# Optimization experiments

Measured on AMD Instinct MI355X. Metric: run time of the kernel, lower is better.

## Reference

```python
import jax, jax.numpy as jnp
import numpy as np

B, S, UNITS = 32, 4096, 512

def setup_inputs() -> dict:
    key = jax.random.key(0)
    ks = jax.random.split(key, 5)
    scale = 1.0 / np.sqrt(UNITS)
    return {
        "s_prev": jax.random.normal(ks[0], (B, UNITS), dtype=jnp.float32),
        "hidden_states": jax.random.normal(ks[1], (B, S, UNITS), dtype=jnp.float32),
        "Ww": jax.random.normal(ks[2], (UNITS, UNITS), dtype=jnp.float32) * scale,
        "Wb": jnp.zeros((UNITS,), dtype=jnp.float32),
        "Uw": jax.random.normal(ks[3], (UNITS, UNITS), dtype=jnp.float32) * scale,
        "Ub": jnp.zeros((UNITS,), dtype=jnp.float32),
        "Vw": jax.random.normal(ks[4], (UNITS, 1), dtype=jnp.float32) * scale,
        "Vb": jnp.zeros((1,), dtype=jnp.float32),
    }

def reference(s_prev, hidden_states, Ww, Wb, Uw, Ub, Vw, Vb):
    # W(s_prev): [B, 1, U] so it broadcasts over seq axis
    W_s = (s_prev @ Ww + Wb)[:, None, :]
    # U(hidden_states): [B, S, U]
    U_h = jnp.einsum('bsu,uv->bsv', hidden_states, Uw) + Ub
    score = jnp.tanh(W_s + U_h)                      # [B, S, U]
    logits = jnp.einsum('bsu,uo->bso', score, Vw) + Vb  # [B, S, 1]
    weights = jax.nn.softmax(logits, axis=1)         # softmax over seq axis
    context = jnp.sum(weights * hidden_states, axis=1)  # [B, U]
    return (context, weights)
```

## Files before the change

kernel.cpp:

```cpp
#include <hip/hip_runtime.h>
#include <hip/hip_bf16.h>

#define UNITS 512
#define SEQ   4096
#define BATCH 32

typedef __attribute__((ext_vector_type(8))) __bf16 bf16x8;
typedef __attribute__((ext_vector_type(4))) __bf16 bf16x4;
typedef __attribute__((ext_vector_type(4))) float  f32x4;

__global__ void k_transpose(const float* __restrict__ Uw, __bf16* __restrict__ UwT) {
    __shared__ float tile[32][33];
    int k0 = blockIdx.x * 32, n0 = blockIdx.y * 32;
    int tx = threadIdx.x, ty = threadIdx.y;
#pragma unroll
    for (int i = 0; i < 4; i++) {
        int k = k0 + ty + i * 8;
        tile[ty + i * 8][tx] = Uw[k * UNITS + n0 + tx];
    }
    __syncthreads();
#pragma unroll
    for (int i = 0; i < 4; i++) {
        int n = n0 + ty + i * 8;
        UwT[n * UNITS + k0 + tx] = (__bf16)tile[tx][ty + i * 8];
    }
}

__global__ void k_wsrow(const float* __restrict__ s_prev, const float* __restrict__ Ww,
                        const float* __restrict__ Wb, const float* __restrict__ Ub,
                        float* __restrict__ ws_Ws) {
    __shared__ float sp[UNITS];
    int b = blockIdx.x, t = threadIdx.x;
    sp[t] = s_prev[b * UNITS + t];
    sp[t + 256] = s_prev[b * UNITS + t + 256];
    __syncthreads();
    float a0 = Wb[t] + Ub[t];
    float a1 = Wb[t + 256] + Ub[t + 256];
#pragma unroll 8
    for (int u = 0; u < UNITS; u++) {
        float s = sp[u];
        a0 += s * Ww[u * UNITS + t];
        a1 += s * Ww[u * UNITS + t + 256];
    }
    ws_Ws[b * UNITS + t] = a0;
    ws_Ws[b * UNITS + t + 256] = a1;
}

#define BM 64
#define BN 256
#define BK 32
#define NSTEP (UNITS / BK)

__launch_bounds__(512)
__global__ void k_logits(const float* __restrict__ hidden, const __bf16* __restrict__ UwT,
                         const float* __restrict__ wsu, const float* __restrict__ Vw,
                         float* __restrict__ lpart) {
    __shared__ __bf16 Ab[2][BM * BK];
    __shared__ __bf16 Bb[2][BN * BK];
    __shared__ float  lred[BM][4];

    const int t = threadIdx.x;
    const int lane = t & 63, wv = t >> 6;
    const int wm = wv >> 2, wn = wv & 3;
    const int l15 = lane & 15, l4 = lane >> 4;
    const int gx = blockIdx.x;
    const int m0 = blockIdx.y * BM;
    const int b  = m0 >> 12;
    const int n0 = gx * BN;

    f32x4 acc[2][4];
#pragma unroll
    for (int i = 0; i < 2; i++)
#pragma unroll
        for (int j = 0; j < 4; j++) acc[i][j] = (f32x4){0.f, 0.f, 0.f, 0.f};

    auto stageA = [&](int buf, int kk) {
        int r = t >> 3, c4 = (t & 7) * 4;
        const float4 v = *(const float4*)(hidden + (size_t)(m0 + r) * UNITS + kk + c4);
        bf16x4 bv;
        bv[0] = (__bf16)v.x; bv[1] = (__bf16)v.y; bv[2] = (__bf16)v.z; bv[3] = (__bf16)v.w;
        *(bf16x4*)(&Ab[buf][r * BK + c4]) = bv;
    };
    auto stageB = [&](int buf, int kk) {
#pragma unroll
        for (int j = 0; j < 2; j++) {
            int idx = wv * 2 + j;
            int nb = idx * 16;
            int n = nb + (lane >> 2);
            int ke = (lane & 3) * 8;
            const __bf16* gp = UwT + (size_t)(n0 + n) * UNITS + kk + ke;
            __builtin_amdgcn_global_load_lds(
                (const __attribute__((address_space(1))) void*)gp,
                (__attribute__((address_space(3))) void*)(&Bb[buf][nb * BK]),
                16, 0, 0);
        }
    };

    stageA(0, 0);
    stageB(0, 0);

#pragma unroll 2
    for (int step = 0; step < NSTEP; ++step) {
        __syncthreads();
        const int cur = step & 1;
        if (step + 1 < NSTEP) {
            stageA(cur ^ 1, (step + 1) * BK);
            stageB(cur ^ 1, (step + 1) * BK);
        }
        bf16x8 a[2], bfr[4];
#pragma unroll
        for (int fi = 0; fi < 2; fi++)
            a[fi] = *(const bf16x8*)(&Ab[cur][(wm * 32 + fi * 16 + l15) * BK + l4 * 8]);
#pragma unroll
        for (int fj = 0; fj < 4; fj++)
            bfr[fj] = *(const bf16x8*)(&Bb[cur][(wn * 64 + fj * 16 + l15) * BK + l4 * 8]);
#pragma unroll
        for (int fi = 0; fi < 2; fi++)
#pragma unroll
            for (int fj = 0; fj < 4; fj++)
                acc[fi][fj] = __builtin_amdgcn_mfma_f32_16x16x32_bf16(a[fi], bfr[fj], acc[fi][fj], 0, 0, 0);
    }

    float wsub[4], vww[4];
#pragma unroll
    for (int fj = 0; fj < 4; fj++) {
        int n = n0 + wn * 64 + fj * 16 + l15;
        wsub[fj] = wsu[b * UNITS + n];
        vww[fj]  = Vw[n];
    }
#pragma unroll
    for (int fi = 0; fi < 2; fi++) {
#pragma unroll
        for (int r = 0; r < 4; r++) {
            float p = 0.f;
#pragma unroll
            for (int fj = 0; fj < 4; fj++) {
                float x = acc[fi][fj][r] + wsub[fj];
                float e = __expf(2.f * x);
                p += vww[fj] * (1.f - 2.f / (e + 1.f));
            }
#pragma unroll
            for (int off = 1; off < 16; off <<= 1) p += __shfl_xor(p, off);
            if (l15 == 0) lred[wm * 32 + fi * 16 + l4 * 4 + r][wn] = p;
        }
    }
    __syncthreads();
    if (t < BM) {
        float s = lred[t][0] + lred[t][1] + lred[t][2] + lred[t][3];
        lpart[(size_t)(m0 + t) * 2 + gx] = s;
    }
}

__global__ void k_softmax(const float* __restrict__ lpart, float* __restrict__ wout) {
    __shared__ float ebuf[SEQ];
    __shared__ float red[8];
    int b = blockIdx.x, t = threadIdx.x;
    int lane = t & 63, wv = t >> 6;
    float m = -1e30f;
#pragma unroll
    for (int i = 0; i < 16; i++) {
        int s = t + i * 256;
        size_t idx = ((size_t)b * SEQ + s) * 2;
        float l = lpart[idx] + lpart[idx + 1];
        ebuf[s] = l;
        m = fmaxf(m, l);
    }
#pragma unroll
    for (int off = 32; off >= 1; off >>= 1) m = fmaxf(m, __shfl_xor(m, off));
    if (lane == 0) red[wv] = m;
    __syncthreads();
    m = fmaxf(fmaxf(red[0], red[1]), fmaxf(red[2], red[3]));
    float zs = 0.f;
#pragma unroll
    for (int i = 0; i < 16; i++) {
        int s = t + i * 256;
        float e = __expf(ebuf[s] - m);
        ebuf[s] = e;
        zs += e;
    }
#pragma unroll
    for (int off = 32; off >= 1; off >>= 1) zs += __shfl_xor(zs, off);
    __syncthreads();
    if (lane == 0) red[wv] = zs;
    __syncthreads();
    float inv = 1.f / (red[0] + red[1] + red[2] + red[3]);
#pragma unroll
    for (int i = 0; i < 16; i++) {
        int s = t + i * 256;
        wout[(size_t)b * SEQ + s] = ebuf[s] * inv;
    }
}

__global__ void k_ctxpart(const float* __restrict__ hidden, const float* __restrict__ wout,
                          float* __restrict__ part) {
    int b = blockIdx.y, c = blockIdx.x, t = threadIdx.x;
    const float* w = wout + (size_t)b * SEQ + c * 128;
    const float* h = hidden + ((size_t)b * SEQ + c * 128) * UNITS;
    float2 acc = make_float2(0.f, 0.f);
#pragma unroll 4
    for (int s = 0; s < 128; s++) {
        float ww = w[s];
        float2 v = ((const float2*)(h + (size_t)s * UNITS))[t];
        acc.x += ww * v.x;
        acc.y += ww * v.y;
    }
    ((float2*)(part + ((size_t)(b * 32 + c)) * UNITS))[t] = acc;
}

__global__ void k_ctxreduce(const float* __restrict__ part, float* __restrict__ ctx) {
    int b = blockIdx.x, t = threadIdx.x;
    float s = 0.f;
#pragma unroll
    for (int c = 0; c < 32; c++) s += part[((size_t)(b * 32 + c)) * UNITS + t];
    ctx[(size_t)b * UNITS + t] = s;
}

extern "C" void kernel_launch(void* const* d_in, const int* in_sizes, int n_in,
                              void* d_out, int out_size, void* d_ws, size_t ws_size,
                              hipStream_t stream) {
    const float* s_prev = (const float*)d_in[0];
    const float* hidden = (const float*)d_in[1];
    const float* Ww     = (const float*)d_in[2];
    const float* Wb     = (const float*)d_in[3];
    const float* Uw     = (const float*)d_in[4];
    const float* Ub     = (const float*)d_in[5];
    const float* Vw     = (const float*)d_in[6];

    float* out  = (float*)d_out;
    float* ctx  = out;
    float* wout = out + BATCH * UNITS;

    float* wsf   = (float*)d_ws;
    float* ws_Ws = wsf;
    float* ws_lp = ws_Ws + BATCH * UNITS;
    float* ws_cp = ws_lp + (size_t)BATCH * SEQ * 2;
    __bf16* UwT  = (__bf16*)(ws_cp + (size_t)BATCH * 32 * UNITS);

    k_transpose<<<dim3(16, 16), dim3(32, 8), 0, stream>>>(Uw, UwT);
    k_wsrow<<<dim3(32), dim3(256), 0, stream>>>(s_prev, Ww, Wb, Ub, ws_Ws);
    k_logits<<<dim3(2, 2048), dim3(512), 0, stream>>>(hidden, UwT, ws_Ws, Vw, ws_lp);
    k_softmax<<<dim3(32), dim3(256), 0, stream>>>(ws_lp, wout);
    k_ctxpart<<<dim3(32, 32), dim3(256), 0, stream>>>(hidden, wout, ws_cp);
    k_ctxreduce<<<dim3(32), dim3(512), 0, stream>>>(ws_cp, ctx);
}
```

Baseline: 225.4 us.

## Double logits M-tile, pre-tile and swizzle Uw, use XOR-swizzled LDS layouts

Doubles the logits GEMM M tile to 128 rows, so each wave computes a 4x4 grid of MFMA fragments and the grid halves. The transposed bf16 Uw is now prepacked into per-k-step, XOR-swizzled 16KB tiles, so the B stage becomes contiguous global_load_lds copies. The A tile is stored with the same swizzle, using 8-element bf16 writes. This is meant to cut redundant reads of hidden, LDS bank conflicts and address arithmetic, at the cost of more registers per thread (launch bounds of 4) and more LDS.

```diff
diff --git a/kernel.cpp b/kernel.cpp
--- a/kernel.cpp
+++ b/kernel.cpp
@@ -6,24 +6,23 @@
 #define BATCH 32
 
 typedef __attribute__((ext_vector_type(8))) __bf16 bf16x8;
-typedef __attribute__((ext_vector_type(4))) __bf16 bf16x4;
 typedef __attribute__((ext_vector_type(4))) float  f32x4;
 
-__global__ void k_transpose(const float* __restrict__ Uw, __bf16* __restrict__ UwT) {
-    __shared__ float tile[32][33];
-    int k0 = blockIdx.x * 32, n0 = blockIdx.y * 32;
-    int tx = threadIdx.x, ty = threadIdx.y;
-#pragma unroll
-    for (int i = 0; i < 4; i++) {
-        int k = k0 + ty + i * 8;
-        tile[ty + i * 8][tx] = Uw[k * UNITS + n0 + tx];
-    }
-    __syncthreads();
-#pragma unroll
-    for (int i = 0; i < 4; i++) {
-        int n = n0 + ty + i * 8;
-        UwT[n * UNITS + k0 + tx] = (__bf16)tile[tx][ty + i * 8];
-    }
+__device__ __forceinline__ int swz(int l) { return l ^ (((l >> 6) & 7) << 4); }
+
+__global__ void k_bprep(const float* __restrict__ Uw, __bf16* __restrict__ UwTt) {
+    const int c     = blockIdx.x;
+    const int half  = blockIdx.y;
+    const int kstep = blockIdx.z;
+    const int t     = threadIdx.x;
+    const int n = half * 256 + t;
+    bf16x8 o;
+#pragma unroll
+    for (int j = 0; j < 8; j++)
+        o[j] = (__bf16)Uw[(size_t)(kstep * 32 + c * 8 + j) * UNITS + n];
+    const int tile = kstep * 2 + half;
+    char* dst = (char*)UwTt + (size_t)tile * 16384 + swz(t * 64 + c * 16);
+    *(bf16x8*)dst = o;
 }
 
 __global__ void k_wsrow(const float* __restrict__ s_prev, const float* __restrict__ Ww,
@@ -46,13 +45,13 @@
     ws_Ws[b * UNITS + t + 256] = a1;
 }
 
-#define BM 64
+#define BM 128
 #define BN 256
 #define BK 32
 #define NSTEP (UNITS / BK)
 
-__launch_bounds__(512)
-__global__ void k_logits(const float* __restrict__ hidden, const __bf16* __restrict__ UwT,
+__launch_bounds__(512, 4)
+__global__ void k_logits(const float* __restrict__ hidden, const __bf16* __restrict__ UwTt,
                          const float* __restrict__ wsu, const float* __restrict__ Vw,
                          float* __restrict__ lpart) {
     __shared__ __bf16 Ab[2][BM * BK];
@@ -66,34 +65,43 @@
     const int gx = blockIdx.x;
     const int m0 = blockIdx.y * BM;
     const int b  = m0 >> 12;
-    const int n0 = gx * BN;
-
-    f32x4 acc[2][4];
-#pragma unroll
-    for (int i = 0; i < 2; i++)
+
+    f32x4 acc[4][4];
+#pragma unroll
+    for (int i = 0; i < 4; i++)
 #pragma unroll
         for (int j = 0; j < 4; j++) acc[i][j] = (f32x4){0.f, 0.f, 0.f, 0.f};
 
+    const int sr = t >> 2;
+    const int sc = t & 3;
+    const float* aRow = hidden + (size_t)(m0 + sr) * UNITS + sc * 8;
+    const int aoffW = swz(sr * 64 + sc * 16);
+
+    int aoffR[4], boffR[4];
+#pragma unroll
+    for (int f = 0; f < 4; f++) {
+        aoffR[f] = swz((wm * 64 + f * 16 + l15) * 64 + l4 * 16);
+        boffR[f] = swz((wn * 64 + f * 16 + l15) * 64 + l4 * 16);
+    }
+
     auto stageA = [&](int buf, int kk) {
-        int r = t >> 3, c4 = (t & 7) * 4;
-        const float4 v = *(const float4*)(hidden + (size_t)(m0 + r) * UNITS + kk + c4);
-        bf16x4 bv;
-        bv[0] = (__bf16)v.x; bv[1] = (__bf16)v.y; bv[2] = (__bf16)v.z; bv[3] = (__bf16)v.w;
-        *(bf16x4*)(&Ab[buf][r * BK + c4]) = bv;
+        float4 v0 = *(const float4*)(aRow + kk);
+        float4 v1 = *(const float4*)(aRow + kk + 4);
+        bf16x8 o;
+        o[0] = (__bf16)v0.x; o[1] = (__bf16)v0.y; o[2] = (__bf16)v0.z; o[3] = (__bf16)v0.w;
+        o[4] = (__bf16)v1.x; o[5] = (__bf16)v1.y; o[6] = (__bf16)v1.z; o[7] = (__bf16)v1.w;
+        *(bf16x8*)((char*)(&Ab[buf][0]) + aoffW) = o;
     };
-    auto stageB = [&](int buf, int kk) {
-#pragma unroll
-        for (int j = 0; j < 2; j++) {
-            int idx = wv * 2 + j;
-            int nb = idx * 16;
-            int n = nb + (lane >> 2);
-            int ke = (lane & 3) * 8;
-            const __bf16* gp = UwT + (size_t)(n0 + n) * UNITS + kk + ke;
-            __builtin_amdgcn_global_load_lds(
-                (const __attribute__((address_space(1))) void*)gp,
-                (__attribute__((address_space(3))) void*)(&Bb[buf][nb * BK]),
-                16, 0, 0);
-        }
+    auto stageB = [&](int buf, int step) {
+        const char* src = (const char*)UwTt + (size_t)(step * 2 + gx) * 16384
+                        + wv * 2048 + lane * 16;
+        char* dst = (char*)(&Bb[buf][0]) + wv * 2048;
+        __builtin_amdgcn_global_load_lds(
+            (const __attribute__((address_space(1))) void*)src,
+            (__attribute__((address_space(3))) void*)dst, 16, 0, 0);
+        __builtin_amdgcn_global_load_lds(
+            (const __attribute__((address_space(1))) void*)(src + 1024),
+            (__attribute__((address_space(3))) void*)(dst + 1024), 16, 0, 0);
     };
 
     stageA(0, 0);
@@ -105,31 +113,31 @@
         const int cur = step & 1;
         if (step + 1 < NSTEP) {
             stageA(cur ^ 1, (step + 1) * BK);
-            stageB(cur ^ 1, (step + 1) * BK);
+            stageB(cur ^ 1, step + 1);
         }
-        bf16x8 a[2], bfr[4];
-#pragma unroll
-        for (int fi = 0; fi < 2; fi++)
-            a[fi] = *(const bf16x8*)(&Ab[cur][(wm * 32 + fi * 16 + l15) * BK + l4 * 8]);
+        bf16x8 a[4], bq[4];
+#pragma unroll
+        for (int fi = 0; fi < 4; fi++)
+            a[fi] = *(const bf16x8*)((char*)(&Ab[cur][0]) + aoffR[fi]);
 #pragma unroll
         for (int fj = 0; fj < 4; fj++)
-            bfr[fj] = *(const bf16x8*)(&Bb[cur][(wn * 64 + fj * 16 + l15) * BK + l4 * 8]);
-#pragma unroll
-        for (int fi = 0; fi < 2; fi++)
+            bq[fj] = *(const bf16x8*)((char*)(&Bb[cur][0]) + boffR[fj]);
+#pragma unroll
+        for (int fi = 0; fi < 4; fi++)
 #pragma unroll
             for (int fj = 0; fj < 4; fj++)
-                acc[fi][fj] = __builtin_amdgcn_mfma_f32_16x16x32_bf16(a[fi], bfr[fj], acc[fi][fj], 0, 0, 0);
+                acc[fi][fj] = __builtin_amdgcn_mfma_f32_16x16x32_bf16(a[fi], bq[fj], acc[fi][fj], 0, 0, 0);
     }
 
     float wsub[4], vww[4];
 #pragma unroll
     for (int fj = 0; fj < 4; fj++) {
-        int n = n0 + wn * 64 + fj * 16 + l15;
+        int n = gx * BN + wn * 64 + fj * 16 + l15;
         wsub[fj] = wsu[b * UNITS + n];
         vww[fj]  = Vw[n];
     }
 #pragma unroll
-    for (int fi = 0; fi < 2; fi++) {
+    for (int fi = 0; fi < 4; fi++) {
 #pragma unroll
         for (int r = 0; r < 4; r++) {
             float p = 0.f;
@@ -141,7 +149,7 @@
             }
 #pragma unroll
             for (int off = 1; off < 16; off <<= 1) p += __shfl_xor(p, off);
-            if (l15 == 0) lred[wm * 32 + fi * 16 + l4 * 4 + r][wn] = p;
+            if (l15 == 0) lred[wm * 64 + fi * 16 + l4 * 4 + r][wn] = p;
         }
     }
     __syncthreads();
@@ -234,11 +242,11 @@
     float* ws_Ws = wsf;
     float* ws_lp = ws_Ws + BATCH * UNITS;
     float* ws_cp = ws_lp + (size_t)BATCH * SEQ * 2;
-    __bf16* UwT  = (__bf16*)(ws_cp + (size_t)BATCH * 32 * UNITS);
-
-    k_transpose<<<dim3(16, 16), dim3(32, 8), 0, stream>>>(Uw, UwT);
+    __bf16* UwTt = (__bf16*)(ws_cp + (size_t)BATCH * 32 * UNITS);
+
+    k_bprep<<<dim3(4, 2, 16), dim3(256), 0, stream>>>(Uw, UwTt);
     k_wsrow<<<dim3(32), dim3(256), 0, stream>>>(s_prev, Ww, Wb, Ub, ws_Ws);
-    k_logits<<<dim3(2, 2048), dim3(512), 0, stream>>>(hidden, UwT, ws_Ws, Vw, ws_lp);
+    k_logits<<<dim3(2, 1024), dim3(512), 0, stream>>>(hidden, UwTt, ws_Ws, Vw, ws_lp);
     k_softmax<<<dim3(32), dim3(256), 0, stream>>>(ws_lp, wout);
     k_ctxpart<<<dim3(32, 32), dim3(256), 0, stream>>>(hidden, wout, ws_cp);
     k_ctxreduce<<<dim3(32), dim3(512), 0, stream>>>(ws_cp, ctx);
```

After: 209.3 us. 1.08x faster.
